# Performance work log

Measured on AMD Instinct MI355X. Metric: run time of the kernel, lower is better.

The kernel has to match this reference:

```python
import jax, jax.numpy as jnp
import numpy as np

B, N, F = 4, 3000, 128

def setup_inputs() -> dict:
    key = jax.random.key(0)
    k1, k2, k3, k4 = jax.random.split(key, 4)
    x = jax.random.normal(k1, (B, N, F), dtype=jnp.float32)
    adj = jax.random.uniform(k2, (B, N, N), dtype=jnp.float32)
    h0 = jax.random.normal(k3, (B, N, F), dtype=jnp.float32)
    stdv = 1.0 / np.sqrt(F)
    theta = jax.random.uniform(k4, (F, F), dtype=jnp.float32, minval=-stdv, maxval=stdv)
    return {
        "x": x, "adj": adj, "h0": h0, "theta": theta,
        "lamda": jnp.float32(0.5), "alpha": jnp.float32(0.1), "l": 4,
    }

def _normalize_adj(adj):
    # add self loops, then D^{-1/2} A D^{-1/2} via elementwise row/col scaling
    # (same math as diag-embed + inverse + two bmms in the original)
    n = adj.shape[1]
    adj = adj + jnp.eye(n, dtype=adj.dtype)
    deg = jnp.sum(adj, axis=2)                      # [B, N]
    d_inv_sqrt = jax.lax.rsqrt(deg)                 # [B, N]
    return d_inv_sqrt[:, :, None] * adj * d_inv_sqrt[:, None, :]

def reference(x, adj, h0, theta, lamda, alpha, l):
    adj_n = _normalize_adj(adj)
    beta = jnp.log(lamda / l + 1.0)
    hi = jnp.einsum('bnm,bmf->bnf', adj_n, x)       # aggregation
    support = (1.0 - alpha) * hi + alpha * h0       # variant=False path
    r = support
    out = beta * jnp.einsum('bnf,fg->bng', support, theta) + (1.0 - beta) * r
    return out
```

## Files before the change

### kernel.cpp

```cpp
#include <hip/hip_runtime.h>
#include <hip/hip_bf16.h>
#include <math.h>

#define BB 4
#define NN 3000
#define FF 128
#define NKC 96
#define NIT 188
#define TS  532

typedef __bf16 bf16x8 __attribute__((ext_vector_type(8)));
typedef __bf16 bf16x4 __attribute__((ext_vector_type(4)));
typedef __bf16 bf16x8a __attribute__((ext_vector_type(8), aligned(8)));
typedef __bf16 bf16x4a __attribute__((ext_vector_type(4), aligned(4)));
typedef float  f32x4  __attribute__((ext_vector_type(4)));

__global__ __launch_bounds__(256) void k_deg(const float* __restrict__ adj,
                                             float* __restrict__ dis) {
    int wid  = (blockIdx.x * 256 + threadIdx.x) >> 6;
    int lane = threadIdx.x & 63;
    if (wid >= BB * NN) return;
    const float4* row = (const float4*)(adj + (size_t)wid * NN);
    float s = 0.f;
    for (int c = lane; c < NN / 4; c += 64) {
        float4 v = row[c];
        s += (v.x + v.y) + (v.z + v.w);
    }
    for (int off = 32; off > 0; off >>= 1) s += __shfl_down(s, off, 64);
    if (lane == 0) dis[wid] = 1.0f / sqrtf(s + 1.0f);
}

__global__ __launch_bounds__(256) void k_xpk(const float* __restrict__ x,
                                             const float* __restrict__ dis,
                                             __bf16* __restrict__ xpk) {
    int b  = blockIdx.y, kc = blockIdx.x;
    int t  = threadIdx.x, w = t >> 6, l = t & 63;
    int m  = l & 15, q = l >> 4;
    #pragma unroll
    for (int h = 0; h < 2; ++h) {
        int nt = w + h * 4;
        int f  = nt * 16 + m;
        bf16x8 v;
        #pragma unroll
        for (int j = 0; j < 8; ++j) {
            int k = kc * 32 + q * 8 + j;
            float val = 0.f;
            if (k < NN) val = dis[b * NN + k] * x[((size_t)b * NN + k) * FF + f];
            v[j] = (__bf16)val;
        }
        *(bf16x8*)(xpk + ((size_t)(b * 8 + nt) * NKC + kc) * 512 + l * 8) = v;
    }
}

__global__ __launch_bounds__(256) void k_thpk(const float* __restrict__ theta,
                                              __bf16* __restrict__ thpk) {
    int kc = blockIdx.x;
    int t  = threadIdx.x, w = t >> 6, l = t & 63;
    int m  = l & 15, q = l >> 4;
    #pragma unroll
    for (int h = 0; h < 2; ++h) {
        int nt = w + h * 4;
        bf16x8 v;
        #pragma unroll
        for (int j = 0; j < 8; ++j) {
            int k = kc * 32 + q * 8 + j;
            v[j] = (__bf16)theta[k * FF + nt * 16 + m];
        }
        *(bf16x8*)(thpk + ((size_t)(nt * 4 + kc)) * 512 + l * 8) = v;
    }
}

__global__ __launch_bounds__(256) void k_agg(const float* __restrict__ adj,
                                             const __bf16* __restrict__ xpk,
                                             const __bf16* __restrict__ thpk,
                                             const float* __restrict__ x,
                                             const float* __restrict__ h0,
                                             const float* __restrict__ dis,
                                             float* __restrict__ out,
                                             const float* __restrict__ alpha_p,
                                             const float* __restrict__ lamda_p,
                                             const int* __restrict__ l_p) {
    __shared__ __bf16 tile[2][16][TS];
    __shared__ __bf16 stile[16][140];
    const int id = blockIdx.x;
    const int b  = (id >> 1) & 3;
    const int it = (id >> 3) * 2 + (id & 1);
    const int i0 = it * 16;
    const int t  = threadIdx.x, w = t >> 6, l = t & 63;
    const int m  = l & 15, quad = l >> 4;
    const int n0 = w * 32;
    const __bf16* B0 = xpk + ((size_t)(b * 8 + 2 * w) * NKC) * 512 + l * 8;
    const __bf16* B1 = B0 + (size_t)NKC * 512;
    f32x4 acc0 = {0.f, 0.f, 0.f, 0.f};
    f32x4 acc1 = {0.f, 0.f, 0.f, 0.f};

    float4 pu[4], pv[4];
    auto load_chunk = [&](int c) {
        #pragma unroll
        for (int i = 0; i < 4; ++i) {
            int row  = i * 4 + w;
            int irow = i0 + row;
            int col  = c * 512 + l * 8;
            float4 u = {0.f, 0.f, 0.f, 0.f}, v = {0.f, 0.f, 0.f, 0.f};
            if (irow < NN && col < NN) {
                const float* p = adj + ((size_t)b * NN + irow) * NN + col;
                u = *(const float4*)p;
                v = *(const float4*)(p + 4);
            }
            pu[i] = u; pv[i] = v;
        }
    };
    auto store_chunk = [&](int cb) {
        #pragma unroll
        for (int i = 0; i < 4; ++i) {
            int row = i * 4 + w;
            bf16x8a s;
            s[0] = (__bf16)pu[i].x; s[1] = (__bf16)pu[i].y;
            s[2] = (__bf16)pu[i].z; s[3] = (__bf16)pu[i].w;
            s[4] = (__bf16)pv[i].x; s[5] = (__bf16)pv[i].y;
            s[6] = (__bf16)pv[i].z; s[7] = (__bf16)pv[i].w;
            *(bf16x8a*)&tile[cb][row][l * 8] = s;
        }
    };

    load_chunk(0);
    store_chunk(0);
    __syncthreads();
    for (int c = 0; c < 6; ++c) {
        int cb = c & 1;
        if (c < 5) load_chunk(c + 1);
        #pragma unroll 4
        for (int kcl = 0; kcl < 16; ++kcl) {
            int kc = c * 16 + kcl;
            bf16x8 a = *(const bf16x8a*)&tile[cb][m][kcl * 32 + quad * 8];
            bf16x8 b0 = *(const bf16x8*)(B0 + (size_t)kc * 512);
            bf16x8 b1 = *(const bf16x8*)(B1 + (size_t)kc * 512);
            acc0 = __builtin_amdgcn_mfma_f32_16x16x32_bf16(a, b0, acc0, 0, 0, 0);
            acc1 = __builtin_amdgcn_mfma_f32_16x16x32_bf16(a, b1, acc1, 0, 0, 0);
        }
        if (c < 5) store_chunk(cb ^ 1);
        __syncthreads();
    }

    const float alpha = *alpha_p;
    const float beta  = logf(*lamda_p / (float)(*l_p) + 1.0f);
    float s0v[4], s1v[4];
    #pragma unroll
    for (int r = 0; r < 4; ++r) {
        int row  = quad * 4 + r;
        int irow = i0 + row;
        float s0 = 0.f, s1 = 0.f;
        if (irow < NN) {
            float  di   = dis[b * NN + irow];
            size_t base = ((size_t)b * NN + irow) * FF;
            int c0 = n0 + m, c1 = n0 + 16 + m;
            s0 = (1.f - alpha) * (di * acc0[r] + di * di * x[base + c0]) + alpha * h0[base + c0];
            s1 = (1.f - alpha) * (di * acc1[r] + di * di * x[base + c1]) + alpha * h0[base + c1];
        }
        s0v[r] = s0; s1v[r] = s1;
        stile[row][n0 + m]      = (__bf16)s0;
        stile[row][n0 + 16 + m] = (__bf16)s1;
    }
    __syncthreads();
    f32x4 o0 = {0.f, 0.f, 0.f, 0.f};
    f32x4 o1 = {0.f, 0.f, 0.f, 0.f};
    const __bf16* T0 = thpk + (size_t)(2 * w * 4) * 512 + l * 8;
    const __bf16* T1 = T0 + 4 * 512;
    #pragma unroll
    for (int kc = 0; kc < 4; ++kc) {
        bf16x4a alo = *(const bf16x4a*)&stile[m][kc * 32 + quad * 8];
        bf16x4a ahi = *(const bf16x4a*)&stile[m][kc * 32 + quad * 8 + 4];
        bf16x8 a = __builtin_shufflevector(alo, ahi, 0, 1, 2, 3, 4, 5, 6, 7);
        bf16x8 tb0 = *(const bf16x8*)(T0 + (size_t)kc * 512);
        bf16x8 tb1 = *(const bf16x8*)(T1 + (size_t)kc * 512);
        o0 = __builtin_amdgcn_mfma_f32_16x16x32_bf16(a, tb0, o0, 0, 0, 0);
        o1 = __builtin_amdgcn_mfma_f32_16x16x32_bf16(a, tb1, o1, 0, 0, 0);
    }
    const float omb = 1.f - beta;
    #pragma unroll
    for (int r = 0; r < 4; ++r) {
        int irow = i0 + quad * 4 + r;
        if (irow < NN) {
            size_t base = ((size_t)b * NN + irow) * FF;
            out[base + n0 + m]      = beta * o0[r] + omb * s0v[r];
            out[base + n0 + 16 + m] = beta * o1[r] + omb * s1v[r];
        }
    }
}

extern "C" void kernel_launch(void* const* d_in, const int* in_sizes, int n_in,
                              void* d_out, int out_size, void* d_ws, size_t ws_size,
                              hipStream_t stream) {
    const float* x      = (const float*)d_in[0];
    const float* adj    = (const float*)d_in[1];
    const float* h0     = (const float*)d_in[2];
    const float* theta  = (const float*)d_in[3];
    const float* lamda  = (const float*)d_in[4];
    const float* alpha  = (const float*)d_in[5];
    const int*   l      = (const int*)d_in[6];
    float* out = (float*)d_out;

    char*   ws   = (char*)d_ws;
    float*  dis  = (float*)ws;
    __bf16* xpk  = (__bf16*)(ws + 65536);
    __bf16* thpk = (__bf16*)(ws + 3276800);

    k_deg<<<dim3((BB * NN) / 4), 256, 0, stream>>>(adj, dis);
    k_thpk<<<dim3(4), 256, 0, stream>>>(theta, thpk);
    k_xpk<<<dim3(NKC, BB), 256, 0, stream>>>(x, dis, xpk);
    k_agg<<<dim3(NIT * BB), 256, 0, stream>>>(adj, xpk, thpk, x, h0, dis, out,
                                              alpha, lamda, l);
}
```

Before: 275.9 us.

## Fuse degree pass with bf16 MFMA-packing of adjacency and stream packed tiles

The degree kernel now also converts each 16-row adjacency tile to bf16 in the MFMA fragment layout and writes it to workspace. A new aggregation kernel reads these packed fragments straight from global memory, with no LDS staging, double buffering or barriers in the main loop. The aim is to replace the second fp32 read of the adjacency with a half-size bf16 read that may stay in the large last-level cache, and to simplify the inner loop. The cost is an extra 72MB workspace write and a dependency on a large workspace; if the workspace is too small the old path is used.

```diff
diff --git a/kernel.cpp b/kernel.cpp
--- a/kernel.cpp
+++ b/kernel.cpp
@@ -14,6 +14,165 @@
 typedef __bf16 bf16x8a __attribute__((ext_vector_type(8), aligned(8)));
 typedef __bf16 bf16x4a __attribute__((ext_vector_type(4), aligned(4)));
 typedef float  f32x4  __attribute__((ext_vector_type(4)));
+
+
+__global__ __launch_bounds__(256) void k_degpk(const float* __restrict__ adj,
+                                               float* __restrict__ dis,
+                                               __bf16* __restrict__ apk) {
+    const int b = blockIdx.y, it = blockIdx.x;
+    const int i0 = it * 16;
+    const int t = threadIdx.x, w = t >> 6, l = t & 63;
+    const int m = l & 15, q = l >> 4;
+    const int irow = i0 + m;
+    const bool rv = irow < NN;
+    const float* arow = adj + ((size_t)b * NN + irow) * NN;
+    __bf16* apt = apk + ((size_t)(b * NIT + it) * NKC) * 512 + l * 8;
+
+    float rsum = 0.f;
+    for (int kc = w; kc < NKC; kc += 4) {
+        int c0 = kc * 32 + q * 8;
+        float4 u = {0.f, 0.f, 0.f, 0.f}, v = {0.f, 0.f, 0.f, 0.f};
+        if (rv && c0 + 8 <= NN) {
+            u = *(const float4*)(arow + c0);
+            v = *(const float4*)(arow + c0 + 4);
+        }
+        rsum += (u.x + u.y) + (u.z + u.w) + (v.x + v.y) + (v.z + v.w);
+        bf16x8 s;
+        s[0] = (__bf16)u.x; s[1] = (__bf16)u.y; s[2] = (__bf16)u.z; s[3] = (__bf16)u.w;
+        s[4] = (__bf16)v.x; s[5] = (__bf16)v.y; s[6] = (__bf16)v.z; s[7] = (__bf16)v.w;
+        *(bf16x8*)(apt + (size_t)kc * 512) = s;
+    }
+    rsum += __shfl_xor(rsum, 16, 64);
+    rsum += __shfl_xor(rsum, 32, 64);
+    __shared__ float ssum[4][16];
+    if (q == 0) ssum[w][m] = rsum;
+    __syncthreads();
+    if (t < 16 && i0 + t < NN) {
+        float tot = ssum[0][t] + ssum[1][t] + ssum[2][t] + ssum[3][t] + 1.0f;
+        dis[b * NN + i0 + t] = 1.0f / sqrtf(tot);
+    }
+}
+
+__global__ __launch_bounds__(256) void k_aggs(const __bf16* __restrict__ apk,
+                                              const __bf16* __restrict__ xpk,
+                                              const __bf16* __restrict__ thpk,
+                                              const float* __restrict__ x,
+                                              const float* __restrict__ h0,
+                                              const float* __restrict__ dis,
+                                              float* __restrict__ out,
+                                              const float* __restrict__ alpha_p,
+                                              const float* __restrict__ lamda_p,
+                                              const int* __restrict__ l_p) {
+    __shared__ __bf16 stile[16][140];
+    const int id = blockIdx.x;
+    const int b  = (id >> 1) & 3;
+    const int it = (id >> 3) * 2 + (id & 1);
+    const int i0 = it * 16;
+    const int t  = threadIdx.x, w = t >> 6, l = t & 63;
+    const int m  = l & 15, quad = l >> 4;
+    const int n0 = w * 32;
+    const __bf16* A0 = apk + ((size_t)(b * NIT + it) * NKC) * 512 + l * 8;
+    const __bf16* B0 = xpk + ((size_t)(b * 8 + 2 * w) * NKC) * 512 + l * 8;
+    const __bf16* B1 = B0 + (size_t)NKC * 512;
+    f32x4 acc0 = {0.f, 0.f, 0.f, 0.f};
+    f32x4 acc1 = {0.f, 0.f, 0.f, 0.f};
+
+    #pragma unroll 8
+    for (int kc = 0; kc < NKC; ++kc) {
+        bf16x8 a  = *(const bf16x8*)(A0 + (size_t)kc * 512);
+        bf16x8 b0 = *(const bf16x8*)(B0 + (size_t)kc * 512);
+        bf16x8 b1 = *(const bf16x8*)(B1 + (size_t)kc * 512);
+        acc0 = __builtin_amdgcn_mfma_f32_16x16x32_bf16(a, b0, acc0, 0, 0, 0);
+        acc1 = __builtin_amdgcn_mfma_f32_16x16x32_bf16(a, b1, acc1, 0, 0, 0);
+    }
+
+    const float alpha = *alpha_p;
+    const float beta  = logf(*lamda_p / (float)(*l_p) + 1.0f);
+    float s0v[4], s1v[4];
+    #pragma unroll
+    for (int r = 0; r < 4; ++r) {
+        int row  = quad * 4 + r;
+        int irow = i0 + row;
+        float s0 = 0.f, s1 = 0.f;
+        if (irow < NN) {
+            float  di   = dis[b * NN + irow];
+            size_t base = ((size_t)b * NN + irow) * FF;
+            int c0 = n0 + m, c1 = n0 + 16 + m;
+            s0 = (1.f - alpha) * (di * acc0[r] + di * di * x[base + c0]) + alpha * h0[base + c0];
+            s1 = (1.f - alpha) * (di * acc1[r] + di * di * x[base + c1]) + alpha * h0[base + c1];
+        }
+        s0v[r] = s0; s1v[r] = s1;
+        stile[row][n0 + m]      = (__bf16)s0;
+        stile[row][n0 + 16 + m] = (__bf16)s1;
+    }
+    __syncthreads();
+    f32x4 o0 = {0.f, 0.f, 0.f, 0.f};
+    f32x4 o1 = {0.f, 0.f, 0.f, 0.f};
+    const __bf16* T0 = thpk + (size_t)(2 * w * 4) * 512 + l * 8;
+    const __bf16* T1 = T0 + 4 * 512;
+    #pragma unroll
+    for (int kc = 0; kc < 4; ++kc) {
+        bf16x4a alo = *(const bf16x4a*)&stile[m][kc * 32 + quad * 8];
+        bf16x4a ahi = *(const bf16x4a*)&stile[m][kc * 32 + quad * 8 + 4];
+        bf16x8 a = __builtin_shufflevector(alo, ahi, 0, 1, 2, 3, 4, 5, 6, 7);
+        bf16x8 tb0 = *(const bf16x8*)(T0 + (size_t)kc * 512);
+        bf16x8 tb1 = *(const bf16x8*)(T1 + (size_t)kc * 512);
+        o0 = __builtin_amdgcn_mfma_f32_16x16x32_bf16(a, tb0, o0, 0, 0, 0);
+        o1 = __builtin_amdgcn_mfma_f32_16x16x32_bf16(a, tb1, o1, 0, 0, 0);
+    }
+    const float omb = 1.f - beta;
+    #pragma unroll
+    for (int r = 0; r < 4; ++r) {
+        int irow = i0 + quad * 4 + r;
+        if (irow < NN) {
+            size_t base = ((size_t)b * NN + irow) * FF;
+            out[base + n0 + m]      = beta * o0[r] + omb * s0v[r];
+            out[base + n0 + 16 + m] = beta * o1[r] + omb * s1v[r];
+        }
+    }
+}
+
+
+__global__ __launch_bounds__(256) void k_xpk(const float* __restrict__ x,
+                                             const float* __restrict__ dis,
+                                             __bf16* __restrict__ xpk) {
+    int b  = blockIdx.y, kc = blockIdx.x;
+    int t  = threadIdx.x, w = t >> 6, l = t & 63;
+    int m  = l & 15, q = l >> 4;
+    #pragma unroll
+    for (int h = 0; h < 2; ++h) {
+        int nt = w + h * 4;
+        int f  = nt * 16 + m;
+        bf16x8 v;
+        #pragma unroll
+        for (int j = 0; j < 8; ++j) {
+            int k = kc * 32 + q * 8 + j;
+            float val = 0.f;
+            if (k < NN) val = dis[b * NN + k] * x[((size_t)b * NN + k) * FF + f];
+            v[j] = (__bf16)val;
+        }
+        *(bf16x8*)(xpk + ((size_t)(b * 8 + nt) * NKC + kc) * 512 + l * 8) = v;
+    }
+}
+
+__global__ __launch_bounds__(256) void k_thpk(const float* __restrict__ theta,
+                                              __bf16* __restrict__ thpk) {
+    int kc = blockIdx.x;
+    int t  = threadIdx.x, w = t >> 6, l = t & 63;
+    int m  = l & 15, q = l >> 4;
+    #pragma unroll
+    for (int h = 0; h < 2; ++h) {
+        int nt = w + h * 4;
+        bf16x8 v;
+        #pragma unroll
+        for (int j = 0; j < 8; ++j) {
+            int k = kc * 32 + q * 8 + j;
+            v[j] = (__bf16)theta[k * FF + nt * 16 + m];
+        }
+        *(bf16x8*)(thpk + ((size_t)(nt * 4 + kc)) * 512 + l * 8) = v;
+    }
+}
+
 
 __global__ __launch_bounds__(256) void k_deg(const float* __restrict__ adj,
                                              float* __restrict__ dis) {
@@ -28,46 +187,6 @@
     }
     for (int off = 32; off > 0; off >>= 1) s += __shfl_down(s, off, 64);
     if (lane == 0) dis[wid] = 1.0f / sqrtf(s + 1.0f);
-}
-
-__global__ __launch_bounds__(256) void k_xpk(const float* __restrict__ x,
-                                             const float* __restrict__ dis,
-                                             __bf16* __restrict__ xpk) {
-    int b  = blockIdx.y, kc = blockIdx.x;
-    int t  = threadIdx.x, w = t >> 6, l = t & 63;
-    int m  = l & 15, q = l >> 4;
-    #pragma unroll
-    for (int h = 0; h < 2; ++h) {
-        int nt = w + h * 4;
-        int f  = nt * 16 + m;
-        bf16x8 v;
-        #pragma unroll
-        for (int j = 0; j < 8; ++j) {
-            int k = kc * 32 + q * 8 + j;
-            float val = 0.f;
-            if (k < NN) val = dis[b * NN + k] * x[((size_t)b * NN + k) * FF + f];
-            v[j] = (__bf16)val;
-        }
-        *(bf16x8*)(xpk + ((size_t)(b * 8 + nt) * NKC + kc) * 512 + l * 8) = v;
-    }
-}
-
-__global__ __launch_bounds__(256) void k_thpk(const float* __restrict__ theta,
-                                              __bf16* __restrict__ thpk) {
-    int kc = blockIdx.x;
-    int t  = threadIdx.x, w = t >> 6, l = t & 63;
-    int m  = l & 15, q = l >> 4;
-    #pragma unroll
-    for (int h = 0; h < 2; ++h) {
-        int nt = w + h * 4;
-        bf16x8 v;
-        #pragma unroll
-        for (int j = 0; j < 8; ++j) {
-            int k = kc * 32 + q * 8 + j;
-            v[j] = (__bf16)theta[k * FF + nt * 16 + m];
-        }
-        *(bf16x8*)(thpk + ((size_t)(nt * 4 + kc)) * 512 + l * 8) = v;
-    }
 }
 
 __global__ __launch_bounds__(256) void k_agg(const float* __restrict__ adj,
@@ -188,6 +307,7 @@
     }
 }
 
+
 extern "C" void kernel_launch(void* const* d_in, const int* in_sizes, int n_in,
                               void* d_out, int out_size, void* d_ws, size_t ws_size,
                               hipStream_t stream) {
@@ -200,14 +320,31 @@
     const int*   l      = (const int*)d_in[6];
     float* out = (float*)d_out;
 
-    char*   ws   = (char*)d_ws;
-    float*  dis  = (float*)ws;
-    __bf16* xpk  = (__bf16*)(ws + 65536);
-    __bf16* thpk = (__bf16*)(ws + 3276800);
-
-    k_deg<<<dim3((BB * NN) / 4), 256, 0, stream>>>(adj, dis);
-    k_thpk<<<dim3(4), 256, 0, stream>>>(theta, thpk);
-    k_xpk<<<dim3(NKC, BB), 256, 0, stream>>>(x, dis, xpk);
-    k_agg<<<dim3(NIT * BB), 256, 0, stream>>>(adj, xpk, thpk, x, h0, dis, out,
-                                              alpha, lamda, l);
-}
+    char* ws = (char*)d_ws;
+
+    const size_t APK_OFF  = 3276800;
+    const size_t WS_NEED  = APK_OFF + (size_t)BB * NIT * NKC * 512 * 2;
+
+    if (ws_size >= WS_NEED) {
+        float*  dis  = (float*)ws;
+        __bf16* thpk = (__bf16*)(ws + 65536);
+        __bf16* xpk  = (__bf16*)(ws + 131072);
+        __bf16* apk  = (__bf16*)(ws + APK_OFF);
+
+        k_degpk<<<dim3(NIT, BB), 256, 0, stream>>>(adj, dis, apk);
+        k_thpk<<<dim3(4), 256, 0, stream>>>(theta, thpk);
+        k_xpk<<<dim3(NKC, BB), 256, 0, stream>>>(x, dis, xpk);
+        k_aggs<<<dim3(NIT * BB), 256, 0, stream>>>(apk, xpk, thpk, x, h0, dis, out,
+                                                   alpha, lamda, l);
+    } else {
+        float*  dis  = (float*)ws;
+        __bf16* xpk  = (__bf16*)(ws + 65536);
+        __bf16* thpk = (__bf16*)(ws + 3276800);
+
+        k_deg<<<dim3((BB * NN) / 4), 256, 0, stream>>>(adj, dis);
+        k_thpk<<<dim3(4), 256, 0, stream>>>(theta, thpk);
+        k_xpk<<<dim3(NKC, BB), 256, 0, stream>>>(x, dis, xpk);
+        k_agg<<<dim3(NIT * BB), 256, 0, stream>>>(adj, xpk, thpk, x, h0, dis, out,
+                                                  alpha, lamda, l);
+    }
+}
```

Measured after the change: 284.1 us. 3.0% more time.
